# Kernel optimization log

Hardware: AMD Instinct MI355X
Metric: run time of the kernel (lower is better)

## Reference

```python
import jax, jax.numpy as jnp
import numpy as np

H = W = 1536
DT = 0.02
FAST_DT, SLOW_DT = 1.0, 0.2
EPS_FAST, EPS_SLOW = 0.06, 0.02
F2S, S2F = 0.04, 0.02


def setup_inputs() -> dict:
    key = jax.random.key(0)
    k1, k2, k3 = jax.random.split(key, 3)
    phi = jax.random.normal(k1, (1, 10, H, W), jnp.float32)
    sensory_map = jax.random.normal(k2, (1, 1, H, W), jnp.float32)
    gamma = jnp.array([0.2, 0.15, 0.1, 0.18, 0.12, 0.13, 0.14, 0.16, 0.11, 0.1], jnp.float32)
    alpha = jnp.array([0.3, 0.25, 0.22, 0.18, 0.2, 0.15, 0.19, 0.24, 0.17, 0.16], jnp.float32)
    mix_w = jax.random.normal(k3, (10, 10), jnp.float32) * 0.1  # 1x1 conv weight, no bias
    return {"phi": phi, "sensory_map": sensory_map, "gamma": gamma, "alpha": alpha, "mix_w": mix_w}


def _lap(x):
    # periodic 5-point Laplacian via rolls on the last two (spatial) dims
    return (jnp.roll(x, 1, -2) + jnp.roll(x, -1, -2)
            + jnp.roll(x, 1, -1) + jnp.roll(x, -1, -1) - 4.0 * x)


def _step(phi, sensory_map, gamma, alpha, mix_w):
    lap = _lap(phi)
    bilap = _lap(lap)
    g, a, p = gamma, alpha, phi
    ch = [
        -g[0] * lap[:, 0] - a[0] * p[:, 0] ** 3 + 0.12 * bilap[:, 0],
        -g[1] * lap[:, 1] + 0.15 * jnp.sin(p[:, 1]) + 0.08 * p[:, 1] ** 3,
        -g[2] * lap[:, 2] + 0.2 * p[:, 2] * (1.0 - p[:, 2] ** 2),
        -g[3] * lap[:, 3] - 0.03 * p[:, 3] ** 5 + 0.08 * bilap[:, 3],
        -g[4] * lap[:, 4] + 0.12 * p[:, 4] * jnp.log(jnp.abs(p[:, 4]) + 1e-6) + 0.02 * bilap[:, 4],
        -g[5] * lap[:, 5] + 0.08 * p[:, 5] ** 3 - 0.02 * p[:, 5] ** 5,
        -g[6] * lap[:, 6] + 0.06 * p[:, 6] ** 4 - 0.04 * p[:, 6],
        -g[7] * lap[:, 7] + 0.08 * jnp.sinh(jnp.clip(p[:, 7], -2.0, 2.0)),
        -g[8] * lap[:, 8] + 0.05 * p[:, 8] ** 2 - 0.08 * p[:, 8],
        -g[9] * lap[:, 9] + 0.02 * p[:, 9] ** 6 - 0.04 * p[:, 9] ** 3 + 0.01 * bilap[:, 9],
    ]
    dphi = jnp.stack(ch, axis=1)                                 # [1,10,H,W]
    coupling = jnp.einsum('oc,bchw->bohw', mix_w, phi)            # 1x1 conv, no bias
    fast_mean = phi[:, :5].mean(axis=1, keepdims=True)            # [1,1,H,W]
    slow_mean = phi[:, 5:].mean(axis=1, keepdims=True)
    sd = sensory_map[:, 0]                                        # [1,H,W]
    dphi_f = dphi[:, :5] + EPS_FAST * coupling[:, :5] + S2F * slow_mean
    dphi_s = dphi[:, 5:] + EPS_SLOW * coupling[:, 5:] + F2S * fast_mean
    dphi_f = dphi_f.at[:, 0].add(0.2 * sd).at[:, 4].add(0.08 * jnp.abs(sd))
    dphi_s = dphi_s.at[:, 4].add(0.05 * sd)                       # global channel 9
    phi_next = jnp.concatenate([phi[:, :5] + DT * FAST_DT * dphi_f,
                                phi[:, 5:] + DT * SLOW_DT * dphi_s], axis=1)
    return jnp.clip(phi_next, -4.0, 4.0)


def reference(phi, sensory_map, gamma, alpha, mix_w):
    phi_next = _step(phi, sensory_map, gamma, alpha, mix_w)
    phi1_mean = phi_next[:, 0].mean(axis=(1, 2))
    phi5_mean = phi_next[:, 4].mean(axis=(1, 2))
    field_means = phi_next.mean(axis=(2, 3))
    return phi_next, phi1_mean, phi5_mean, field_means
```

## Files before the change

kernel.cpp:

```cpp
#include <hip/hip_runtime.h>
#include <math.h>

#define HH 1536
#define WW 1536
#define HWSZ (HH*WW)
#define NT 384

__device__ __forceinline__ float4 LD4(const float* __restrict__ p, int row, int t) {
    return reinterpret_cast<const float4*>(p + row)[t];
}

__global__ __launch_bounds__(NT) void step_kernel(
    const float* __restrict__ phi,
    const float* __restrict__ sensory,
    const float* __restrict__ gamma,
    const float* __restrict__ alpha,
    const float* __restrict__ mixw,
    float* __restrict__ out,
    float* __restrict__ sums)
{
    __shared__ float s_mix[100];
    __shared__ float s_g[10];
    __shared__ float s_a0;
    __shared__ float s_red[6][10];

    const int tid = threadIdx.x;
    if (tid < 100) s_mix[tid] = mixw[tid];
    if (tid < 10)  s_g[tid]   = gamma[tid];
    if (tid == 0)  s_a0       = alpha[0];
    __syncthreads();

    const int blk = blockIdx.x;
    const int y = (blk & 7) * 192 + (blk >> 3);

    const int x0 = tid * 4;

    const int ym1 = (y == 0)      ? HH - 1     : y - 1;
    const int yp1 = (y == HH - 1) ? 0          : y + 1;
    const int ym2 = (y < 2)       ? y + HH - 2 : y - 2;
    const int yp2 = (y >= HH - 2) ? y - HH + 2 : y + 2;

    const int r0  = y   * WW;
    const int rm1 = ym1 * WW;
    const int rp1 = yp1 * WW;
    const int rm2 = ym2 * WW;
    const int rp2 = yp2 * WW;

    const int xl1 = (x0 == 0)        ? WW - 1 : x0 - 1;
    const int xl2 = (x0 == 0)        ? WW - 2 : x0 - 2;
    const int xr1 = (x0 + 4 == WW)   ? 0      : x0 + 4;
    const int xr2 = (x0 + 4 == WW)   ? 1      : x0 + 5;

    float pv[10][4];
    float dv[10][4];

    #pragma unroll
    for (int c = 0; c < 10; ++c) {
        const float* pc = phi + (size_t)c * HWSZ;
        const float4 cm = LD4(pc, r0,  tid);
        const float4 nn = LD4(pc, rm1, tid);
        const float4 ss = LD4(pc, rp1, tid);
        const float wl1 = pc[r0 + xl1];
        const float wr1 = pc[r0 + xr1];

        float lap[4];
        lap[0] = nn.x + ss.x + wl1  + cm.y - 4.0f * cm.x;
        lap[1] = nn.y + ss.y + cm.x + cm.z - 4.0f * cm.y;
        lap[2] = nn.z + ss.z + cm.y + cm.w - 4.0f * cm.z;
        lap[3] = nn.w + ss.w + cm.z + wr1  - 4.0f * cm.w;

        float bl[4] = {0.f, 0.f, 0.f, 0.f};
        if (c == 0 || c == 3 || c == 4 || c == 9) {
            const float4 t2n = LD4(pc, rm2, tid);
            const float4 t2s = LD4(pc, rp2, tid);
            const float wl2 = pc[r0  + xl2];
            const float wr2 = pc[r0  + xr2];
            const float nwl = pc[rm1 + xl1];
            const float ner = pc[rm1 + xr1];
            const float swl = pc[rp1 + xl1];
            const float ser = pc[rp1 + xr1];
            bl[0] = 20.0f*cm.x - 8.0f*(nn.x + ss.x + wl1  + cm.y)
                  + 2.0f*(nwl  + nn.y + swl  + ss.y) + (t2n.x + t2s.x + wl2  + cm.z);
            bl[1] = 20.0f*cm.y - 8.0f*(nn.y + ss.y + cm.x + cm.z)
                  + 2.0f*(nn.x + nn.z + ss.x + ss.z) + (t2n.y + t2s.y + wl1  + cm.w);
            bl[2] = 20.0f*cm.z - 8.0f*(nn.z + ss.z + cm.y + cm.w)
                  + 2.0f*(nn.y + nn.w + ss.y + ss.w) + (t2n.z + t2s.z + cm.x + wr1);
            bl[3] = 20.0f*cm.w - 8.0f*(nn.w + ss.w + cm.z + wr1)
                  + 2.0f*(nn.z + ner  + ss.z + ser ) + (t2n.w + t2s.w + cm.y + wr2);
        }

        pv[c][0] = cm.x; pv[c][1] = cm.y; pv[c][2] = cm.z; pv[c][3] = cm.w;

        #pragma unroll
        for (int k = 0; k < 4; ++k) {
            const float pp = pv[c][k];
            const float lv = lap[k];
            const float bv = bl[k];
            float dd;
            switch (c) {
            case 0: dd = -s_g[0]*lv - s_a0*pp*pp*pp + 0.12f*bv; break;
            case 1: dd = -s_g[1]*lv + 0.15f*sinf(pp) + 0.08f*pp*pp*pp; break;
            case 2: dd = -s_g[2]*lv + 0.2f*pp*(1.0f - pp*pp); break;
            case 3: { const float p2 = pp*pp;
                      dd = -s_g[3]*lv - 0.03f*p2*p2*pp + 0.08f*bv; } break;
            case 4: dd = -s_g[4]*lv + 0.12f*pp*logf(fabsf(pp) + 1e-6f) + 0.02f*bv; break;
            case 5: { const float p2 = pp*pp;
                      dd = -s_g[5]*lv + 0.08f*p2*pp - 0.02f*p2*p2*pp; } break;
            case 6: { const float p2 = pp*pp;
                      dd = -s_g[6]*lv + 0.06f*p2*p2 - 0.04f*pp; } break;
            case 7: { const float pc7 = fminf(fmaxf(pp, -2.0f), 2.0f);
                      dd = -s_g[7]*lv + 0.08f*sinhf(pc7); } break;
            case 8: dd = -s_g[8]*lv + 0.05f*pp*pp - 0.08f*pp; break;
            default: { const float p3 = pp*pp*pp;
                       dd = -s_g[9]*lv + 0.02f*p3*p3 - 0.04f*p3 + 0.01f*bv; } break;
            }
            dv[c][k] = dd;
        }
    }

    float fmv[4], smv[4], sdk[4];
    {
        const float4 sd4 = LD4(sensory, r0, tid);
        sdk[0] = sd4.x; sdk[1] = sd4.y; sdk[2] = sd4.z; sdk[3] = sd4.w;
        #pragma unroll
        for (int k = 0; k < 4; ++k) {
            fmv[k] = (pv[0][k] + pv[1][k] + pv[2][k] + pv[3][k] + pv[4][k]) * 0.2f;
            smv[k] = (pv[5][k] + pv[6][k] + pv[7][k] + pv[8][k] + pv[9][k]) * 0.2f;
        }
    }

    const int lane = tid & 63;
    const int wave = tid >> 6;

    #pragma unroll
    for (int o = 0; o < 10; ++o) {
        float pn[4];
        #pragma unroll
        for (int k = 0; k < 4; ++k) {
            float cp = 0.0f;
            #pragma unroll
            for (int c = 0; c < 10; ++c) cp = fmaf(s_mix[o*10 + c], pv[c][k], cp);
            float dd = dv[o][k];
            if (o < 5) {
                dd += 0.06f * cp + 0.02f * smv[k];
                if (o == 0) dd += 0.2f  * sdk[k];
                if (o == 4) dd += 0.08f * fabsf(sdk[k]);
                pn[k] = pv[o][k] + 0.02f * dd;
            } else {
                dd += 0.02f * cp + 0.04f * fmv[k];
                if (o == 9) dd += 0.05f * sdk[k];
                pn[k] = pv[o][k] + 0.004f * dd;
            }
            pn[k] = fminf(fmaxf(pn[k], -4.0f), 4.0f);
        }
        float4 o4; o4.x = pn[0]; o4.y = pn[1]; o4.z = pn[2]; o4.w = pn[3];
        reinterpret_cast<float4*>(out + (size_t)o * HWSZ + r0)[tid] = o4;

        float s = pn[0] + pn[1] + pn[2] + pn[3];
        #pragma unroll
        for (int off = 32; off > 0; off >>= 1) s += __shfl_down(s, off, 64);
        if (lane == 0) s_red[wave][o] = s;
    }

    __syncthreads();
    if (tid < 10) {
        float v = 0.0f;
        #pragma unroll
        for (int w = 0; w < 6; ++w) v += s_red[w][tid];
        atomicAdd(&sums[tid], v);
    }
}

__global__ void finalize_kernel(const float* __restrict__ sums,
                                float* __restrict__ out)
{
    const int t = threadIdx.x;
    const float inv = 1.0f / (float)HWSZ;
    const size_t base = (size_t)10 * HWSZ;
    if (t == 0) out[base]     = sums[0] * inv;
    if (t == 1) out[base + 1] = sums[4] * inv;
    if (t >= 2 && t < 12) out[base + 2 + (t - 2)] = sums[t - 2] * inv;
}

extern "C" void kernel_launch(void* const* d_in, const int* in_sizes, int n_in,
                              void* d_out, int out_size, void* d_ws, size_t ws_size,
                              hipStream_t stream) {
    const float* phi     = (const float*)d_in[0];
    const float* sensory = (const float*)d_in[1];
    const float* gamma   = (const float*)d_in[2];
    const float* alpha   = (const float*)d_in[3];
    const float* mixw    = (const float*)d_in[4];
    float* out = (float*)d_out;
    float* sums = (float*)d_ws;

    hipMemsetAsync(sums, 0, 10 * sizeof(float), stream);

    step_kernel<<<dim3(HH), NT, 0, stream>>>(phi, sensory, gamma, alpha, mixw, out, sums);
    finalize_kernel<<<1, 64, 0, stream>>>(sums, out);
}
```

Measured before the change: 241.7 us.

## Use 256-thread wave-segment blocks, shuffle halos, fast intrinsics and vectorized mix loads

Switches from one 384-thread block per row to 256-thread blocks where each wave handles a 64-float4 segment of a row, with launch bounds requesting higher occupancy. Horizontal halo values now come from wave shuffles, and only edge lanes issue scalar global loads. Gamma and alpha are read into registers, and the mix weights are padded in shared memory and read as vectors. sin, log and sinh are replaced with fast intrinsics, which changes numerical accuracy slightly.

```diff
diff --git a/kernel.cpp b/kernel.cpp
--- a/kernel.cpp
+++ b/kernel.cpp
@@ -4,13 +4,15 @@
 #define HH 1536
 #define WW 1536
 #define HWSZ (HH*WW)
-#define NT 384
-
-__device__ __forceinline__ float4 LD4(const float* __restrict__ p, int row, int t) {
-    return reinterpret_cast<const float4*>(p + row)[t];
-}
-
-__global__ __launch_bounds__(NT) void step_kernel(
+#define NT 256
+#define NBLK ((HH*WW/4)/NT)
+#define BPX (NBLK/8)
+
+__device__ __forceinline__ float4 LD4(const float* __restrict__ p, int row, int idx) {
+    return reinterpret_cast<const float4*>(p + row)[idx];
+}
+
+__global__ __launch_bounds__(NT, 4) void step_kernel(
     const float* __restrict__ phi,
     const float* __restrict__ sensory,
     const float* __restrict__ gamma,
@@ -19,21 +21,22 @@
     float* __restrict__ out,
     float* __restrict__ sums)
 {
-    __shared__ float s_mix[100];
-    __shared__ float s_g[10];
-    __shared__ float s_a0;
-    __shared__ float s_red[6][10];
+    __shared__ float s_mix[10][12];
+    __shared__ float s_red[4][10];
 
     const int tid = threadIdx.x;
-    if (tid < 100) s_mix[tid] = mixw[tid];
-    if (tid < 10)  s_g[tid]   = gamma[tid];
-    if (tid == 0)  s_a0       = alpha[0];
-    __syncthreads();
-
-    const int blk = blockIdx.x;
-    const int y = (blk & 7) * 192 + (blk >> 3);
-
-    const int x0 = tid * 4;
+    if (tid < 100) s_mix[tid / 10][tid % 10] = mixw[tid];
+
+    const int b  = blockIdx.x;
+    const int nb = (b & 7) * BPX + (b >> 3);
+
+    const int lane = tid & 63;
+    const int wave = tid >> 6;
+    const int gw   = nb * 4 + wave;
+    const int y    = gw / 6;
+    const int wseg = gw - y * 6;
+    const int col  = wseg * 64 + lane;
+    const int x0   = col * 4;
 
     const int ym1 = (y == 0)      ? HH - 1     : y - 1;
     const int yp1 = (y == HH - 1) ? 0          : y + 1;
@@ -46,10 +49,14 @@
     const int rm2 = ym2 * WW;
     const int rp2 = yp2 * WW;
 
-    const int xl1 = (x0 == 0)        ? WW - 1 : x0 - 1;
-    const int xl2 = (x0 == 0)        ? WW - 2 : x0 - 2;
-    const int xr1 = (x0 + 4 == WW)   ? 0      : x0 + 4;
-    const int xr2 = (x0 + 4 == WW)   ? 1      : x0 + 5;
+    const int xl1 = (x0 == 0)      ? WW - 1 : x0 - 1;
+    const int xl2 = (x0 == 0)      ? WW - 2 : x0 - 2;
+    const int xr1 = (x0 + 4 == WW) ? 0      : x0 + 4;
+    const int xr2 = (x0 + 4 == WW) ? 1      : x0 + 5;
+
+    const float g0 = gamma[0], g1 = gamma[1], g2 = gamma[2], g3 = gamma[3], g4 = gamma[4];
+    const float g5 = gamma[5], g6 = gamma[6], g7 = gamma[7], g8 = gamma[8], g9 = gamma[9];
+    const float a0 = alpha[0];
 
     float pv[10][4];
     float dv[10][4];
@@ -57,11 +64,34 @@
     #pragma unroll
     for (int c = 0; c < 10; ++c) {
         const float* pc = phi + (size_t)c * HWSZ;
-        const float4 cm = LD4(pc, r0,  tid);
-        const float4 nn = LD4(pc, rm1, tid);
-        const float4 ss = LD4(pc, rp1, tid);
-        const float wl1 = pc[r0 + xl1];
-        const float wr1 = pc[r0 + xr1];
+        const float4 cm = LD4(pc, r0,  col);
+        const float4 nn = LD4(pc, rm1, col);
+        const float4 ss = LD4(pc, rp1, col);
+
+        float wl1 = __shfl_up  (cm.w, 1, 64);
+        float wr1 = __shfl_down(cm.x, 1, 64);
+
+        const bool BI = (c == 0 || c == 3 || c == 4 || c == 9);
+        float4 t2n = {0,0,0,0}, t2s = {0,0,0,0};
+        float wl2 = 0.f, wr2 = 0.f, nwl = 0.f, ner = 0.f, swl = 0.f, ser = 0.f;
+        if (BI) {
+            t2n = LD4(pc, rm2, col);
+            t2s = LD4(pc, rp2, col);
+            wl2 = __shfl_up  (cm.z, 1, 64);
+            wr2 = __shfl_down(cm.y, 1, 64);
+            nwl = __shfl_up  (nn.w, 1, 64);
+            ner = __shfl_down(nn.x, 1, 64);
+            swl = __shfl_up  (ss.w, 1, 64);
+            ser = __shfl_down(ss.x, 1, 64);
+        }
+        if (lane == 0) {
+            wl1 = pc[r0 + xl1];
+            if (BI) { wl2 = pc[r0 + xl2]; nwl = pc[rm1 + xl1]; swl = pc[rp1 + xl1]; }
+        }
+        if (lane == 63) {
+            wr1 = pc[r0 + xr1];
+            if (BI) { wr2 = pc[r0 + xr2]; ner = pc[rm1 + xr1]; ser = pc[rp1 + xr1]; }
+        }
 
         float lap[4];
         lap[0] = nn.x + ss.x + wl1  + cm.y - 4.0f * cm.x;
@@ -70,15 +100,7 @@
         lap[3] = nn.w + ss.w + cm.z + wr1  - 4.0f * cm.w;
 
         float bl[4] = {0.f, 0.f, 0.f, 0.f};
-        if (c == 0 || c == 3 || c == 4 || c == 9) {
-            const float4 t2n = LD4(pc, rm2, tid);
-            const float4 t2s = LD4(pc, rp2, tid);
-            const float wl2 = pc[r0  + xl2];
-            const float wr2 = pc[r0  + xr2];
-            const float nwl = pc[rm1 + xl1];
-            const float ner = pc[rm1 + xr1];
-            const float swl = pc[rp1 + xl1];
-            const float ser = pc[rp1 + xr1];
+        if (BI) {
             bl[0] = 20.0f*cm.x - 8.0f*(nn.x + ss.x + wl1  + cm.y)
                   + 2.0f*(nwl  + nn.y + swl  + ss.y) + (t2n.x + t2s.x + wl2  + cm.z);
             bl[1] = 20.0f*cm.y - 8.0f*(nn.y + ss.y + cm.x + cm.z)
@@ -98,21 +120,23 @@
             const float bv = bl[k];
             float dd;
             switch (c) {
-            case 0: dd = -s_g[0]*lv - s_a0*pp*pp*pp + 0.12f*bv; break;
-            case 1: dd = -s_g[1]*lv + 0.15f*sinf(pp) + 0.08f*pp*pp*pp; break;
-            case 2: dd = -s_g[2]*lv + 0.2f*pp*(1.0f - pp*pp); break;
+            case 0: dd = -g0*lv - a0*pp*pp*pp + 0.12f*bv; break;
+            case 1: dd = -g1*lv + 0.15f*__sinf(pp) + 0.08f*pp*pp*pp; break;
+            case 2: dd = -g2*lv + 0.2f*pp*(1.0f - pp*pp); break;
             case 3: { const float p2 = pp*pp;
-                      dd = -s_g[3]*lv - 0.03f*p2*p2*pp + 0.08f*bv; } break;
-            case 4: dd = -s_g[4]*lv + 0.12f*pp*logf(fabsf(pp) + 1e-6f) + 0.02f*bv; break;
+                      dd = -g3*lv - 0.03f*p2*p2*pp + 0.08f*bv; } break;
+            case 4: dd = -g4*lv + 0.12f*pp*__logf(fabsf(pp) + 1e-6f) + 0.02f*bv; break;
             case 5: { const float p2 = pp*pp;
-                      dd = -s_g[5]*lv + 0.08f*p2*pp - 0.02f*p2*p2*pp; } break;
+                      dd = -g5*lv + 0.08f*p2*pp - 0.02f*p2*p2*pp; } break;
             case 6: { const float p2 = pp*pp;
-                      dd = -s_g[6]*lv + 0.06f*p2*p2 - 0.04f*pp; } break;
+                      dd = -g6*lv + 0.06f*p2*p2 - 0.04f*pp; } break;
             case 7: { const float pc7 = fminf(fmaxf(pp, -2.0f), 2.0f);
-                      dd = -s_g[7]*lv + 0.08f*sinhf(pc7); } break;
-            case 8: dd = -s_g[8]*lv + 0.05f*pp*pp - 0.08f*pp; break;
+                      const float ex  = __expf(pc7);
+                      const float exm = __expf(-pc7);
+                      dd = -g7*lv + 0.04f*(ex - exm); } break;
+            case 8: dd = -g8*lv + 0.05f*pp*pp - 0.08f*pp; break;
             default: { const float p3 = pp*pp*pp;
-                       dd = -s_g[9]*lv + 0.02f*p3*p3 - 0.04f*p3 + 0.01f*bv; } break;
+                       dd = -g9*lv + 0.02f*p3*p3 - 0.04f*p3 + 0.01f*bv; } break;
             }
             dv[c][k] = dd;
         }
@@ -120,7 +144,7 @@
 
     float fmv[4], smv[4], sdk[4];
     {
-        const float4 sd4 = LD4(sensory, r0, tid);
+        const float4 sd4 = LD4(sensory, r0, col);
         sdk[0] = sd4.x; sdk[1] = sd4.y; sdk[2] = sd4.z; sdk[3] = sd4.w;
         #pragma unroll
         for (int k = 0; k < 4; ++k) {
@@ -129,17 +153,27 @@
         }
     }
 
-    const int lane = tid & 63;
-    const int wave = tid >> 6;
+    __syncthreads();
 
     #pragma unroll
     for (int o = 0; o < 10; ++o) {
+        const float4 m0 = *reinterpret_cast<const float4*>(&s_mix[o][0]);
+        const float4 m1 = *reinterpret_cast<const float4*>(&s_mix[o][4]);
+        const float2 m2 = *reinterpret_cast<const float2*>(&s_mix[o][8]);
         float pn[4];
         #pragma unroll
         for (int k = 0; k < 4; ++k) {
-            float cp = 0.0f;
-            #pragma unroll
-            for (int c = 0; c < 10; ++c) cp = fmaf(s_mix[o*10 + c], pv[c][k], cp);
+            float cp;
+            cp = m0.x * pv[0][k];
+            cp = fmaf(m0.y, pv[1][k], cp);
+            cp = fmaf(m0.z, pv[2][k], cp);
+            cp = fmaf(m0.w, pv[3][k], cp);
+            cp = fmaf(m1.x, pv[4][k], cp);
+            cp = fmaf(m1.y, pv[5][k], cp);
+            cp = fmaf(m1.z, pv[6][k], cp);
+            cp = fmaf(m1.w, pv[7][k], cp);
+            cp = fmaf(m2.x, pv[8][k], cp);
+            cp = fmaf(m2.y, pv[9][k], cp);
             float dd = dv[o][k];
             if (o < 5) {
                 dd += 0.06f * cp + 0.02f * smv[k];
@@ -154,7 +188,7 @@
             pn[k] = fminf(fmaxf(pn[k], -4.0f), 4.0f);
         }
         float4 o4; o4.x = pn[0]; o4.y = pn[1]; o4.z = pn[2]; o4.w = pn[3];
-        reinterpret_cast<float4*>(out + (size_t)o * HWSZ + r0)[tid] = o4;
+        reinterpret_cast<float4*>(out + (size_t)o * HWSZ + r0)[col] = o4;
 
         float s = pn[0] + pn[1] + pn[2] + pn[3];
         #pragma unroll
@@ -164,9 +198,7 @@
 
     __syncthreads();
     if (tid < 10) {
-        float v = 0.0f;
-        #pragma unroll
-        for (int w = 0; w < 6; ++w) v += s_red[w][tid];
+        float v = s_red[0][tid] + s_red[1][tid] + s_red[2][tid] + s_red[3][tid];
         atomicAdd(&sums[tid], v);
     }
 }
@@ -195,6 +227,6 @@
 
     hipMemsetAsync(sums, 0, 10 * sizeof(float), stream);
 
-    step_kernel<<<dim3(HH), NT, 0, stream>>>(phi, sensory, gamma, alpha, mixw, out, sums);
+    step_kernel<<<dim3(NBLK), NT, 0, stream>>>(phi, sensory, gamma, alpha, mixw, out, sums);
     finalize_kernel<<<1, 64, 0, stream>>>(sums, out);
 }
```

After: 297.8 us. 23.2% more time.
